# Performance work log

Measured on AMD Instinct MI355X. Metric: run time of the kernel, lower is better.

The kernel has to match this reference:

```python
import jax, jax.numpy as jnp
import numpy as np

B, L, N, T, D, V, C = 128, 512, 1023, 511, 256, 50000, 511
EPS = 1e-6


def circular_correlation(a, b):
    # c_k = sum_i a_i * b_{(i+k) mod d}  == irfft(conj(rfft(a)) * rfft(b))
    d = a.shape[-1]
    c = jnp.fft.irfft(jnp.conj(jnp.fft.rfft(a, axis=-1)) * jnp.fft.rfft(b, axis=-1), n=d, axis=-1)
    return c / (jnp.linalg.norm(c, axis=-1, keepdims=True) + EPS)


def setup_inputs() -> dict:
    key = jax.random.key(0)
    k1, k2, k3, k4, k5, k6, k7, k8 = jax.random.split(key, 8)
    num_node = jnp.full((B,), N, dtype=jnp.int64 if jax.config.jax_enable_x64 else jnp.int32)
    # leaf slot index: leaves occupy node slots 0..L-1 (deterministic, no scatter collisions)
    slot = jnp.broadcast_to(jnp.arange(L, dtype=jnp.int32)[None, :], (B, L))
    vocab_id = jax.random.randint(k1, (B, L), 0, V, dtype=jnp.int32)
    leaf_content_id = jnp.stack([slot, vocab_id], axis=-1)  # [B, L, 2]
    content_mask = (jax.random.uniform(k2, (B, L)) < 0.9).astype(jnp.int32)
    ctype = jax.random.randint(k3, (B, T), 0, 3, dtype=jnp.int32)          # 0 = no-op, 1, 2 children
    parent = jax.random.randint(k4, (B, T), L, N, dtype=jnp.int32)         # internal node slots
    lchild = jax.random.randint(k5, (B, T), 0, N, dtype=jnp.int32)
    rchild = jax.random.randint(k6, (B, T), 0, N, dtype=jnp.int32)
    composition_info = jnp.stack([ctype, parent, lchild, rchild], axis=-1)  # [B, T, 4]
    emb_weight = jax.random.normal(k7, (V, D), dtype=jnp.float32) * 0.1
    lin_weight = jax.random.normal(k8, (C, D), dtype=jnp.float32) * 0.05
    lin_bias = jnp.zeros((C,), dtype=jnp.float32)
    return {"num_node": num_node, "leaf_content_id": leaf_content_id,
            "content_mask": content_mask, "composition_info": composition_info,
            "emb_weight": emb_weight, "lin_weight": lin_weight, "lin_bias": lin_bias}


def embed_leaf_nodes(leaf_content_id, content_mask, emb_weight):
    leaf_vec = emb_weight[leaf_content_id[:, :, 1]]          # [B, L, D]
    node_idx = leaf_content_id[:, :, 0]                      # [B, L]
    mask = content_mask != 0
    safe_idx = jnp.where(mask, node_idx, N)                  # N is out-of-bounds -> dropped
    vec = jnp.zeros((B, N, D), dtype=leaf_vec.dtype)
    vec = vec.at[jnp.arange(B)[:, None], safe_idx].set(leaf_vec, mode="drop")
    norm = jnp.linalg.norm(vec, axis=2, keepdims=True) + EPS
    return vec / norm


def compose(vec, composition_info):
    bidx = jnp.arange(B)

    def step(v, info):  # info: [B, 4] for one tree level
        t, p, l, r = info[:, 0], info[:, 1], info[:, 2], info[:, 3]
        safe_p = jnp.where(t > 0, p, 0)
        lv = v[bidx, l]                                      # [B, D]
        rv = v[bidx, r]
        two = circular_correlation(lv, rv)
        cur = v[bidx, safe_p]
        val = jnp.where((t == 1)[:, None], lv,
                        jnp.where((t == 2)[:, None], two, cur))
        return v.at[bidx, safe_p].set(val), None

    vec, _ = jax.lax.scan(step, vec, jnp.swapaxes(composition_info, 0, 1))
    return vec


def reference(num_node, leaf_content_id, content_mask, composition_info,
              emb_weight, lin_weight, lin_bias):
    vec = embed_leaf_nodes(leaf_content_id, content_mask, emb_weight)
    vec = compose(vec, composition_info)
    out = jnp.einsum("bnd,cd->bnc", vec, lin_weight) + lin_bias
    return out
```

## Files before the change

kernel.cpp:

```cpp
#include <hip/hip_runtime.h>

#define NB 128
#define NL 512
#define NN 1023
#define NT 511
#define ND 256
#define NC 511
#define EPSF 1e-6f

#define SRC_ZERO (-1)
#define SLOTC 4096
#define STEPC 8192

typedef __attribute__((ext_vector_type(8))) short short8;
typedef __attribute__((ext_vector_type(4))) float f32x4;
typedef __attribute__((ext_vector_type(2))) float f32x2;

__device__ __forceinline__ unsigned short f2bf(float f) {
  unsigned u = __builtin_bit_cast(unsigned, f);
  u += 0x7FFFu + ((u >> 16) & 1u);
  return (unsigned short)(u >> 16);
}

__global__ void __launch_bounds__(256) embed_scatter(
    const int* __restrict__ lcid, const int* __restrict__ cmask,
    const float* __restrict__ emb, const float* __restrict__ lw,
    float* __restrict__ leafbuf, unsigned short* __restrict__ vecb,
    unsigned short* __restrict__ wb) {
  if (blockIdx.x >= 16384) {
    int i   = (blockIdx.x - 16384) * 256 + threadIdx.x;
    int row = i >> 5;
    uint4 r = {0u, 0u, 0u, 0u};
    if (row < NC) {
      const float4* v4 = (const float4*)lw;
      float4 x = v4[2 * i], y = v4[2 * i + 1];
      r.x = (unsigned)f2bf(x.x) | ((unsigned)f2bf(x.y) << 16);
      r.y = (unsigned)f2bf(x.z) | ((unsigned)f2bf(x.w) << 16);
      r.z = (unsigned)f2bf(y.x) | ((unsigned)f2bf(y.y) << 16);
      r.w = (unsigned)f2bf(y.z) | ((unsigned)f2bf(y.w) << 16);
    }
    ((uint4*)wb)[i] = r;
    return;
  }
  int rid  = blockIdx.x * 4 + (threadIdx.x >> 6);
  int lane = threadIdx.x & 63;
  int slot = lcid[2 * rid];
  int vid  = lcid[2 * rid + 1];
  int msk  = cmask[rid];
  int b    = rid >> 9;
  float4 v = {0.f, 0.f, 0.f, 0.f};
  if (msk) v = ((const float4*)(emb + (size_t)vid * ND))[lane];
  float ss = v.x * v.x + v.y * v.y + v.z * v.z + v.w * v.w;
#pragma unroll
  for (int off = 32; off > 0; off >>= 1) ss += __shfl_down(ss, off, 64);
  ss = __shfl(ss, 0, 64);
  float inv = 1.0f / (sqrtf(ss) + EPSF);
  float4 o;
  o.x = v.x * inv; o.y = v.y * inv; o.z = v.z * inv; o.w = v.w * inv;
  ((float4*)(leafbuf + ((size_t)b * 512 + slot) * ND))[lane] = o;
  uint2 pk;
  pk.x = (unsigned)f2bf(o.x) | ((unsigned)f2bf(o.y) << 16);
  pk.y = (unsigned)f2bf(o.z) | ((unsigned)f2bf(o.w) << 16);
  ((uint2*)(vecb + ((size_t)b * NN + slot) * ND))[lane] = pk;
}

__global__ void __launch_bounds__(1024) compose_kernel(
    const int* __restrict__ info, const int* __restrict__ lcid,
    const int* __restrict__ cmask, const float* __restrict__ leafbuf,
    float* __restrict__ outbuf, int* __restrict__ fsrcG) {
  const int b    = blockIdx.x;
  const int tid  = threadIdx.x;
  const int lane = tid & 63;
  const int wav  = tid >> 6;

  __shared__ int4 sinfo4[NT];
  __shared__ int ptr_[NT];
  __shared__ int lsA[NT], rsA[NT];
  __shared__ int lvl[NT], fsrc[NT];
  __shared__ int schedS[NT], schedL[NT], schedR[NT];
  __shared__ int offs[512], cnt[512], cnt2[512];
  __shared__ unsigned char deadF[NT], liveF[NT], lzero[512];
  __shared__ float a_st[16][256];
  __shared__ float b_st[16][512];
  __shared__ float s_st[16][512];
  __shared__ int changed, smax;

  const float* lb = leafbuf + (size_t)b * 512 * ND;
  float*       ob = outbuf + (size_t)b * NT * ND;

  const int4* ib4 = (const int4*)(info + (size_t)b * NT * 4);
  for (int i = tid; i < NT; i += 1024) sinfo4[i] = ib4[i];
  if (tid < 512) lzero[tid] = 1;
  if (tid == 0) smax = 0;
  __syncthreads();
  if (tid < NL) {
    int row = lcid[((size_t)b * NL + tid) * 2];
    lzero[row] = (cmask[(size_t)b * NL + tid] == 0) ? 1 : 0;
  }
  __syncthreads();

  const int t = tid;
  int4 m1 = {0, 0, 0, 0};
  if (t < NT) m1 = sinfo4[t];
  int l1 = -1, r1 = -1, f1 = -1;
  const int prow = 512 + t;
  for (int tp = 0; tp < NT; ++tp) {
    int4 wi = sinfo4[tp];
    if (wi.x > 0) {
      if (t < NT && tp < t) { if (wi.y == m1.z) l1 = tp; if (wi.y == m1.w) r1 = tp; }
      if (wi.y == prow) f1 = tp;
    }
  }
  __syncthreads();

  if (t < NT) {
    int v;
    if (m1.x == 2) v = SLOTC + t;
    else if (m1.x == 1) {
      if (m1.z < 512) v = m1.z;
      else v = (l1 >= 0) ? (STEPC + l1) : SRC_ZERO;
    } else v = SRC_ZERO;
    ptr_[t] = v;
  }
  __syncthreads();
  for (int it = 0; it < 10; ++it) {
    int v = 0;
    if (t < NT) { v = ptr_[t]; if (v >= STEPC) v = ptr_[v - STEPC]; }
    __syncthreads();
    if (t < NT) ptr_[t] = v;
    __syncthreads();
  }

  auto normv = [&](int v) -> int {
    if (v >= 0 && v < 512 && lzero[v]) return SRC_ZERO;
    return v;
  };
  auto collapseW = [&](int wstep) -> int {
    int v = (sinfo4[wstep].x == 2) ? (SLOTC + wstep) : ptr_[wstep];
    return normv(v);
  };
  if (t < NT) {
    if (m1.x == 2) {
      int a = (m1.z < 512) ? normv(m1.z) : ((l1 >= 0) ? collapseW(l1) : SRC_ZERO);
      int c = (m1.w < 512) ? normv(m1.w) : ((r1 >= 0) ? collapseW(r1) : SRC_ZERO);
      lsA[t] = a; rsA[t] = c;
      deadF[t] = (a == SRC_ZERO || c == SRC_ZERO) ? 1 : 0;
    } else {
      deadF[t] = 0;
    }
    liveF[t] = 0;
    fsrc[t] = (f1 >= 0) ? collapseW(f1) : SRC_ZERO;
  }
  __syncthreads();

  for (int rounds = 0; rounds < NT; ++rounds) {
    if (tid == 0) changed = 0;
    __syncthreads();
    if (t < NT && m1.x == 2 && !deadF[t]) {
      int a = lsA[t], c = rsA[t];
      if (a >= SLOTC && deadF[a - SLOTC]) { a = SRC_ZERO; lsA[t] = a; }
      if (c >= SLOTC && deadF[c - SLOTC]) { c = SRC_ZERO; rsA[t] = c; }
      if (a == SRC_ZERO || c == SRC_ZERO) { deadF[t] = 1; changed = 1; }
    }
    __syncthreads();
    if (!changed) break;
    __syncthreads();
  }

  if (t < NT) {
    int f = fsrc[t];
    if (f >= SLOTC && deadF[f - SLOTC]) { f = SRC_ZERO; fsrc[t] = f; }
    if (f >= SLOTC) liveF[f - SLOTC] = 1;
  }
  __syncthreads();
  for (int rounds = 0; rounds < NT; ++rounds) {
    if (tid == 0) changed = 0;
    __syncthreads();
    if (t < NT && m1.x == 2 && liveF[t] && !deadF[t]) {
      int a = lsA[t], c = rsA[t];
      if (a >= SLOTC && !liveF[a - SLOTC]) { liveF[a - SLOTC] = 1; changed = 1; }
      if (c >= SLOTC && !liveF[c - SLOTC]) { liveF[c - SLOTC] = 1; changed = 1; }
    }
    __syncthreads();
    if (!changed) break;
    __syncthreads();
  }

  const bool isLive = (t < NT && m1.x == 2 && liveF[t] && !deadF[t]);

  if (t < NT) lvl[t] = 0;
  __syncthreads();
  for (int rounds = 0; rounds < NT; ++rounds) {
    if (tid == 0) changed = 0;
    __syncthreads();
    if (isLive) {
      int nl = 1, a = lsA[t], c = rsA[t];
      if (a >= SLOTC) { int dl = lvl[a - SLOTC] + 1; if (dl > nl) nl = dl; }
      if (c >= SLOTC) { int dl = lvl[c - SLOTC] + 1; if (dl > nl) nl = dl; }
      if (nl > lvl[t]) { lvl[t] = nl; changed = 1; }
    }
    __syncthreads();
    if (!changed) break;
    __syncthreads();
  }
  if (isLive) atomicMax(&smax, lvl[t]);

  if (tid < 512) { cnt[tid] = 0; cnt2[tid] = 0; }
  __syncthreads();
  if (isLive) atomicAdd(&cnt[lvl[t]], 1);
  __syncthreads();
  if (tid < 512) offs[tid] = cnt[tid];
  __syncthreads();
  for (int k = 1; k < 512; k <<= 1) {
    int v = 0;
    if (tid < 512) { v = offs[tid]; if (tid >= k) v += offs[tid - k]; }
    __syncthreads();
    if (tid < 512) offs[tid] = v;
    __syncthreads();
  }
  if (isLive) {
    int d = lvl[t];
    int pos = offs[d - 1] + atomicAdd(&cnt2[d], 1);
    schedS[pos] = t; schedL[pos] = lsA[t]; schedR[pos] = rsA[t];
  }
  __syncthreads();

  const int maxd = smax;
  for (int d = 1; d <= maxd; ++d) {
    const int base = offs[d - 1];
    const int nops = cnt[d];
    const int nch  = (nops + 15) >> 4;
    for (int ch = 0; ch < nch; ++ch) {
      int rel = ch * 16 + wav;
      if (rel < nops) {
        int my = base + rel;
        int tt = schedS[my], ls = schedL[my], rs = schedR[my];
        const float* pa = (ls < 512) ? lb + (size_t)ls * ND
                                     : ob + (size_t)(ls - SLOTC) * ND;
        const float* pb = (rs < 512) ? lb + (size_t)rs * ND
                                     : ob + (size_t)(rs - SLOTC) * ND;
        float4 av = ((const float4*)pa)[lane];
        float4 bv = ((const float4*)pb)[lane];
        float nx = __shfl(bv.x, (lane + 1) & 63, 64);
        float4 sv = {bv.y, bv.z, bv.w, nx};
        ((float4*)a_st[wav])[lane]      = av;
        ((float4*)b_st[wav])[lane]      = bv;
        ((float4*)b_st[wav])[lane + 64] = bv;
        ((float4*)s_st[wav])[lane]      = sv;
        ((float4*)s_st[wav])[lane + 64] = sv;
        const float4* a4 = (const float4*)a_st[wav];
        const float4* b4 = (const float4*)b_st[wav];
        const float4* s4 = (const float4*)s_st[wav];
        f32x2 q0 = {0.f, 0.f}, q1 = {0.f, 0.f}, q2 = {0.f, 0.f}, q3 = {0.f, 0.f};
        float4 B0 = b4[lane];
        float4 S0 = s4[lane];
#pragma unroll 8
        for (int i = 0; i < 64; ++i) {
          float4 A  = a4[i];
          float4 B1 = b4[lane + i + 1];
          float4 S1 = s4[lane + i + 1];
          f32x2 Axy = {A.x, A.y},  Azw = {A.z, A.w};
          f32x2 Bxy = {B0.x, B0.y}, Bzw = {B0.z, B0.w};
          f32x2 Sxy = {S0.x, S0.y}, Szw = {S0.z, S0.w};
          f32x2 B1xy = {B1.x, B1.y}, S1xy = {S1.x, S1.y};
          q0 += Axy * Bxy;  q0 += Azw * Bzw;
          q1 += Axy * Sxy;  q1 += Azw * Szw;
          q2 += Axy * Bzw;  q2 += Azw * B1xy;
          q3 += Axy * Szw;  q3 += Azw * S1xy;
          B0 = B1; S0 = S1;
        }
        float c0 = q0.x + q0.y, c1 = q1.x + q1.y;
        float c2 = q2.x + q2.y, c3 = q3.x + q3.y;
        float ss = c0 * c0 + c1 * c1 + c2 * c2 + c3 * c3;
#pragma unroll
        for (int off = 32; off > 0; off >>= 1) ss += __shfl_down(ss, off, 64);
        ss = __shfl(ss, 0, 64);
        float inv = 1.f / (sqrtf(ss) + EPSF);
        float4 res;
        res.x = c0 * inv; res.y = c1 * inv; res.z = c2 * inv; res.w = c3 * inv;
        ((float4*)(ob + (size_t)tt * ND))[lane] = res;
      }
    }
    __syncthreads();
  }

  for (int i = tid; i < NT; i += 1024) fsrcG[b * NT + i] = fsrc[i];
}

__global__ void __launch_bounds__(256) gather_rows(
    const int* __restrict__ fsrcG, const float* __restrict__ leafbuf,
    const float* __restrict__ outbuf, unsigned short* __restrict__ vecb) {
  int rid  = blockIdx.x * 4 + (threadIdx.x >> 6);
  int lane = threadIdx.x & 63;
  int b    = rid / NT;
  int idx  = rid - b * NT;
  int s    = fsrcG[rid];
  float4 v = {0.f, 0.f, 0.f, 0.f};
  if (s >= 0) {
    const float* src = (s < 512)
        ? (leafbuf + ((size_t)b * 512 + s) * ND)
        : (outbuf + ((size_t)b * NT + (s - SLOTC)) * ND);
    v = ((const float4*)src)[lane];
  }
  uint2 pk;
  pk.x = (unsigned)f2bf(v.x) | ((unsigned)f2bf(v.y) << 16);
  pk.y = (unsigned)f2bf(v.z) | ((unsigned)f2bf(v.w) << 16);
  ((uint2*)(vecb + ((size_t)b * NN + 512 + idx) * ND))[lane] = pk;
}

union GemmSh {
  struct { short As[128 * 64]; short Ws[128 * 64]; } s;
  float epi[4][16][65];
};

__global__ void __launch_bounds__(256) gemm_kernel(
    const short* __restrict__ A, const short* __restrict__ W,
    const float* __restrict__ bias, float* __restrict__ out) {
  __shared__ GemmSh sh;
  int i = blockIdx.x;
  int m = (i >> 5) * 8 + (i & 7);
  int c = (i >> 3) & 3;
  if (m >= 1023) return;
  int tid  = threadIdx.x;
  int lane = tid & 63;
  int w    = tid >> 6;
  int c0   = c * 128;
  int m0   = m * 128;
  int wm   = (w & 1) * 64;
  int wc   = (w >> 1) * 64;
  int frow = lane & 15;
  int quad = lane >> 4;
  f32x4 acc[4][4];
#pragma unroll
  for (int a = 0; a < 4; ++a)
#pragma unroll
    for (int j = 0; j < 4; ++j) acc[a][j] = (f32x4){0.f, 0.f, 0.f, 0.f};

  for (int k0 = 0; k0 < ND; k0 += 64) {
#pragma unroll
    for (int a = 0; a < 4; ++a) {
      int idx = a * 256 + tid;
      int row = idx >> 3;
      int ch  = idx & 7;
      int chs = ch ^ (row & 7);
      const short* ga = A + (size_t)(m0 + row) * ND + k0 + chs * 8;
      const short* gw = W + (size_t)(c0 + row) * ND + k0 + chs * 8;
      __builtin_amdgcn_global_load_lds(
          (const __attribute__((address_space(1))) void*)ga,
          (__attribute__((address_space(3))) void*)(sh.s.As + idx * 8), 16, 0, 0);
      __builtin_amdgcn_global_load_lds(
          (const __attribute__((address_space(1))) void*)gw,
          (__attribute__((address_space(3))) void*)(sh.s.Ws + idx * 8), 16, 0, 0);
    }
    __syncthreads();
#pragma unroll
    for (int ks = 0; ks < 2; ++ks) {
      short8 af[4], wf[4];
#pragma unroll
      for (int mi = 0; mi < 4; ++mi) {
        int r = wm + mi * 16 + frow;
        int cc = (ks * 4 + quad) ^ (r & 7);
        af[mi] = *(const short8*)(sh.s.As + r * 64 + cc * 8);
      }
#pragma unroll
      for (int ci = 0; ci < 4; ++ci) {
        int r = wc + ci * 16 + frow;
        int cc = (ks * 4 + quad) ^ (r & 7);
        wf[ci] = *(const short8*)(sh.s.Ws + r * 64 + cc * 8);
      }
#pragma unroll
      for (int mi = 0; mi < 4; ++mi)
#pragma unroll
        for (int ci = 0; ci < 4; ++ci)
          acc[mi][ci] = __builtin_amdgcn_mfma_f32_16x16x32_bf16(
              af[mi], wf[ci], acc[mi][ci], 0, 0, 0);
    }
    __syncthreads();
  }

  int colg = c0 + wc + lane;
  float bv = (colg < NC) ? bias[colg] : 0.f;
#pragma unroll
  for (int mi = 0; mi < 4; ++mi) {
#pragma unroll
    for (int ci = 0; ci < 4; ++ci)
#pragma unroll
      for (int r = 0; r < 4; ++r)
        sh.epi[w][quad * 4 + r][ci * 16 + frow] = acc[mi][ci][r];
    if (colg < NC) {
      int mrow = m0 + wm + mi * 16;
#pragma unroll
      for (int rr = 0; rr < 16; ++rr)
        out[(size_t)(mrow + rr) * NC + colg] = sh.epi[w][rr][lane] + bv;
    }
  }
}

extern "C" void kernel_launch(void* const* d_in, const int* in_sizes, int n_in,
                              void* d_out, int out_size, void* d_ws, size_t ws_size,
                              hipStream_t stream) {
  const int*   lcid  = (const int*)d_in[1];
  const int*   cmask = (const int*)d_in[2];
  const int*   cinfo = (const int*)d_in[3];
  const float* emb   = (const float*)d_in[4];
  const float* lw    = (const float*)d_in[5];
  const float* lbias = (const float*)d_in[6];
  float*       out   = (float*)d_out;

  char* ws = (char*)d_ws;
  float*          leafbuf = (float*)ws;
  float*          outbuf  = (float*)(ws + 67108864);
  unsigned short* vecb    = (unsigned short*)(ws + 134086656);
  unsigned short* wb      = (unsigned short*)(ws + 201129984);
  int*            fsrcG   = (int*)d_out;

  embed_scatter<<<16448, 256, 0, stream>>>(lcid, cmask, emb, lw,
                                           leafbuf, vecb, wb);
  compose_kernel<<<NB, 1024, 0, stream>>>(cinfo, lcid, cmask, leafbuf,
                                          outbuf, fsrcG);
  gather_rows<<<NB * NT / 4, 256, 0, stream>>>(fsrcG, leafbuf, outbuf, vecb);
  gemm_kernel<<<4096, 256, 0, stream>>>(
      (const short*)vecb, (const short*)wb, lbias, out);
}
```

Measured before the change: 520.6 us.

## Overlap leaf-row GEMM with tree composition in a fused kernel

The compose kernel gains 1024 extra blocks that compute the output projection for the leaf rows (slots 0..511), whose bf16 vectors are already final after the embed step. These blocks fill the GPU while the 128 compose blocks run their serial dependency walk. The later GEMM now covers only the internal-node rows, which halves its grid. The fsrc scratch is moved inside the output buffer to a region that only the second GEMM writes. This relies on compose blocks being scheduled first, and the fused kernel keeps 1024-thread blocks with the large union shared-memory footprint, which can limit occupancy for the GEMM blocks.

```diff
diff --git a/kernel.cpp b/kernel.cpp
--- a/kernel.cpp
+++ b/kernel.cpp
@@ -64,227 +64,323 @@
   ((uint2*)(vecb + ((size_t)b * NN + slot) * ND))[lane] = pk;
 }
 
-__global__ void __launch_bounds__(1024) compose_kernel(
+struct ComposeSh {
+  int4 sinfo4[NT];
+  int ptr_[NT];
+  int lsA[NT], rsA[NT];
+  int lvl[NT], fsrc[NT];
+  int schedS[NT], schedL[NT], schedR[NT];
+  int offs[512], cnt[512], cnt2[512];
+  unsigned char deadF[NT], liveF[NT], lzero[512];
+  float a_st[16][256];
+  float b_st[16][512];
+  float s_st[16][512];
+  int changed, smax;
+};
+struct LeafGemmSh { short As[256 * 64]; short Ws[128 * 64]; };
+union FuseSh { ComposeSh c; LeafGemmSh g; };
+
+__global__ void __launch_bounds__(1024) compose_leafgemm(
     const int* __restrict__ info, const int* __restrict__ lcid,
     const int* __restrict__ cmask, const float* __restrict__ leafbuf,
-    float* __restrict__ outbuf, int* __restrict__ fsrcG) {
-  const int b    = blockIdx.x;
+    float* __restrict__ outbuf, int* __restrict__ fsrcG,
+    const short* __restrict__ vecbS, const short* __restrict__ wbs,
+    const float* __restrict__ bias, float* __restrict__ out) {
+  __shared__ FuseSh sh;
   const int tid  = threadIdx.x;
   const int lane = tid & 63;
   const int wav  = tid >> 6;
 
-  __shared__ int4 sinfo4[NT];
-  __shared__ int ptr_[NT];
-  __shared__ int lsA[NT], rsA[NT];
-  __shared__ int lvl[NT], fsrc[NT];
-  __shared__ int schedS[NT], schedL[NT], schedR[NT];
-  __shared__ int offs[512], cnt[512], cnt2[512];
-  __shared__ unsigned char deadF[NT], liveF[NT], lzero[512];
-  __shared__ float a_st[16][256];
-  __shared__ float b_st[16][512];
-  __shared__ float s_st[16][512];
-  __shared__ int changed, smax;
-
-  const float* lb = leafbuf + (size_t)b * 512 * ND;
-  float*       ob = outbuf + (size_t)b * NT * ND;
-
-  const int4* ib4 = (const int4*)(info + (size_t)b * NT * 4);
-  for (int i = tid; i < NT; i += 1024) sinfo4[i] = ib4[i];
-  if (tid < 512) lzero[tid] = 1;
-  if (tid == 0) smax = 0;
-  __syncthreads();
-  if (tid < NL) {
-    int row = lcid[((size_t)b * NL + tid) * 2];
-    lzero[row] = (cmask[(size_t)b * NL + tid] == 0) ? 1 : 0;
-  }
-  __syncthreads();
-
-  const int t = tid;
-  int4 m1 = {0, 0, 0, 0};
-  if (t < NT) m1 = sinfo4[t];
-  int l1 = -1, r1 = -1, f1 = -1;
-  const int prow = 512 + t;
-  for (int tp = 0; tp < NT; ++tp) {
-    int4 wi = sinfo4[tp];
-    if (wi.x > 0) {
-      if (t < NT && tp < t) { if (wi.y == m1.z) l1 = tp; if (wi.y == m1.w) r1 = tp; }
-      if (wi.y == prow) f1 = tp;
-    }
-  }
-  __syncthreads();
-
-  if (t < NT) {
-    int v;
-    if (m1.x == 2) v = SLOTC + t;
-    else if (m1.x == 1) {
-      if (m1.z < 512) v = m1.z;
-      else v = (l1 >= 0) ? (STEPC + l1) : SRC_ZERO;
-    } else v = SRC_ZERO;
-    ptr_[t] = v;
-  }
-  __syncthreads();
-  for (int it = 0; it < 10; ++it) {
-    int v = 0;
-    if (t < NT) { v = ptr_[t]; if (v >= STEPC) v = ptr_[v - STEPC]; }
-    __syncthreads();
-    if (t < NT) ptr_[t] = v;
-    __syncthreads();
-  }
-
-  auto normv = [&](int v) -> int {
-    if (v >= 0 && v < 512 && lzero[v]) return SRC_ZERO;
-    return v;
-  };
-  auto collapseW = [&](int wstep) -> int {
-    int v = (sinfo4[wstep].x == 2) ? (SLOTC + wstep) : ptr_[wstep];
-    return normv(v);
-  };
-  if (t < NT) {
-    if (m1.x == 2) {
-      int a = (m1.z < 512) ? normv(m1.z) : ((l1 >= 0) ? collapseW(l1) : SRC_ZERO);
-      int c = (m1.w < 512) ? normv(m1.w) : ((r1 >= 0) ? collapseW(r1) : SRC_ZERO);
-      lsA[t] = a; rsA[t] = c;
-      deadF[t] = (a == SRC_ZERO || c == SRC_ZERO) ? 1 : 0;
-    } else {
-      deadF[t] = 0;
-    }
-    liveF[t] = 0;
-    fsrc[t] = (f1 >= 0) ? collapseW(f1) : SRC_ZERO;
-  }
-  __syncthreads();
-
-  for (int rounds = 0; rounds < NT; ++rounds) {
-    if (tid == 0) changed = 0;
-    __syncthreads();
-    if (t < NT && m1.x == 2 && !deadF[t]) {
-      int a = lsA[t], c = rsA[t];
-      if (a >= SLOTC && deadF[a - SLOTC]) { a = SRC_ZERO; lsA[t] = a; }
-      if (c >= SLOTC && deadF[c - SLOTC]) { c = SRC_ZERO; rsA[t] = c; }
-      if (a == SRC_ZERO || c == SRC_ZERO) { deadF[t] = 1; changed = 1; }
-    }
-    __syncthreads();
-    if (!changed) break;
-    __syncthreads();
-  }
-
-  if (t < NT) {
-    int f = fsrc[t];
-    if (f >= SLOTC && deadF[f - SLOTC]) { f = SRC_ZERO; fsrc[t] = f; }
-    if (f >= SLOTC) liveF[f - SLOTC] = 1;
-  }
-  __syncthreads();
-  for (int rounds = 0; rounds < NT; ++rounds) {
-    if (tid == 0) changed = 0;
-    __syncthreads();
-    if (t < NT && m1.x == 2 && liveF[t] && !deadF[t]) {
-      int a = lsA[t], c = rsA[t];
-      if (a >= SLOTC && !liveF[a - SLOTC]) { liveF[a - SLOTC] = 1; changed = 1; }
-      if (c >= SLOTC && !liveF[c - SLOTC]) { liveF[c - SLOTC] = 1; changed = 1; }
-    }
-    __syncthreads();
-    if (!changed) break;
-    __syncthreads();
-  }
-
-  const bool isLive = (t < NT && m1.x == 2 && liveF[t] && !deadF[t]);
-
-  if (t < NT) lvl[t] = 0;
-  __syncthreads();
-  for (int rounds = 0; rounds < NT; ++rounds) {
-    if (tid == 0) changed = 0;
-    __syncthreads();
+  if (blockIdx.x < NB) {
+    const int b = blockIdx.x;
+    int4 (&sinfo4)[NT] = sh.c.sinfo4;
+    int (&ptr_)[NT] = sh.c.ptr_;
+    int (&lsA)[NT] = sh.c.lsA;  int (&rsA)[NT] = sh.c.rsA;
+    int (&lvl)[NT] = sh.c.lvl;  int (&fsrc)[NT] = sh.c.fsrc;
+    int (&schedS)[NT] = sh.c.schedS; int (&schedL)[NT] = sh.c.schedL;
+    int (&schedR)[NT] = sh.c.schedR;
+    int (&offs)[512] = sh.c.offs; int (&cnt)[512] = sh.c.cnt;
+    int (&cnt2)[512] = sh.c.cnt2;
+    unsigned char (&deadF)[NT] = sh.c.deadF;
+    unsigned char (&liveF)[NT] = sh.c.liveF;
+    unsigned char (&lzero)[512] = sh.c.lzero;
+    float (&a_st)[16][256] = sh.c.a_st;
+    float (&b_st)[16][512] = sh.c.b_st;
+    float (&s_st)[16][512] = sh.c.s_st;
+    int &changed = sh.c.changed; int &smax = sh.c.smax;
+
+    const float* lb = leafbuf + (size_t)b * 512 * ND;
+    float*       ob = outbuf + (size_t)b * NT * ND;
+
+    const int4* ib4 = (const int4*)(info + (size_t)b * NT * 4);
+    for (int i = tid; i < NT; i += 1024) sinfo4[i] = ib4[i];
+    if (tid < 512) lzero[tid] = 1;
+    if (tid == 0) smax = 0;
+    __syncthreads();
+    if (tid < NL) {
+      int row = lcid[((size_t)b * NL + tid) * 2];
+      lzero[row] = (cmask[(size_t)b * NL + tid] == 0) ? 1 : 0;
+    }
+    __syncthreads();
+
+    const int t = tid;
+    int4 m1 = {0, 0, 0, 0};
+    if (t < NT) m1 = sinfo4[t];
+    int l1 = -1, r1 = -1, f1 = -1;
+    const int prow = 512 + t;
+    for (int tp = 0; tp < NT; ++tp) {
+      int4 wi = sinfo4[tp];
+      if (wi.x > 0) {
+        if (t < NT && tp < t) { if (wi.y == m1.z) l1 = tp; if (wi.y == m1.w) r1 = tp; }
+        if (wi.y == prow) f1 = tp;
+      }
+    }
+    __syncthreads();
+
+    if (t < NT) {
+      int v;
+      if (m1.x == 2) v = SLOTC + t;
+      else if (m1.x == 1) {
+        if (m1.z < 512) v = m1.z;
+        else v = (l1 >= 0) ? (STEPC + l1) : SRC_ZERO;
+      } else v = SRC_ZERO;
+      ptr_[t] = v;
+    }
+    __syncthreads();
+    for (int it = 0; it < 10; ++it) {
+      int v = 0;
+      if (t < NT) { v = ptr_[t]; if (v >= STEPC) v = ptr_[v - STEPC]; }
+      __syncthreads();
+      if (t < NT) ptr_[t] = v;
+      __syncthreads();
+    }
+
+    auto normv = [&](int v) -> int {
+      if (v >= 0 && v < 512 && lzero[v]) return SRC_ZERO;
+      return v;
+    };
+    auto collapseW = [&](int wstep) -> int {
+      int v = (sinfo4[wstep].x == 2) ? (SLOTC + wstep) : ptr_[wstep];
+      return normv(v);
+    };
+    if (t < NT) {
+      if (m1.x == 2) {
+        int a = (m1.z < 512) ? normv(m1.z) : ((l1 >= 0) ? collapseW(l1) : SRC_ZERO);
+        int c = (m1.w < 512) ? normv(m1.w) : ((r1 >= 0) ? collapseW(r1) : SRC_ZERO);
+        lsA[t] = a; rsA[t] = c;
+        deadF[t] = (a == SRC_ZERO || c == SRC_ZERO) ? 1 : 0;
+      } else {
+        deadF[t] = 0;
+      }
+      liveF[t] = 0;
+      fsrc[t] = (f1 >= 0) ? collapseW(f1) : SRC_ZERO;
+    }
+    __syncthreads();
+
+    for (int rounds = 0; rounds < NT; ++rounds) {
+      if (tid == 0) changed = 0;
+      __syncthreads();
+      if (t < NT && m1.x == 2 && !deadF[t]) {
+        int a = lsA[t], c = rsA[t];
+        if (a >= SLOTC && deadF[a - SLOTC]) { a = SRC_ZERO; lsA[t] = a; }
+        if (c >= SLOTC && deadF[c - SLOTC]) { c = SRC_ZERO; rsA[t] = c; }
+        if (a == SRC_ZERO || c == SRC_ZERO) { deadF[t] = 1; changed = 1; }
+      }
+      __syncthreads();
+      if (!changed) break;
+      __syncthreads();
+    }
+
+    if (t < NT) {
+      int f = fsrc[t];
+      if (f >= SLOTC && deadF[f - SLOTC]) { f = SRC_ZERO; fsrc[t] = f; }
+      if (f >= SLOTC) liveF[f - SLOTC] = 1;
+    }
+    __syncthreads();
+    for (int rounds = 0; rounds < NT; ++rounds) {
+      if (tid == 0) changed = 0;
+      __syncthreads();
+      if (t < NT && m1.x == 2 && liveF[t] && !deadF[t]) {
+        int a = lsA[t], c = rsA[t];
+        if (a >= SLOTC && !liveF[a - SLOTC]) { liveF[a - SLOTC] = 1; changed = 1; }
+        if (c >= SLOTC && !liveF[c - SLOTC]) { liveF[c - SLOTC] = 1; changed = 1; }
+      }
+      __syncthreads();
+      if (!changed) break;
+      __syncthreads();
+    }
+
+    const bool isLive = (t < NT && m1.x == 2 && liveF[t] && !deadF[t]);
+
+    if (t < NT) lvl[t] = 0;
+    __syncthreads();
+    for (int rounds = 0; rounds < NT; ++rounds) {
+      if (tid == 0) changed = 0;
+      __syncthreads();
+      if (isLive) {
+        int nl = 1, a = lsA[t], c = rsA[t];
+        if (a >= SLOTC) { int dl = lvl[a - SLOTC] + 1; if (dl > nl) nl = dl; }
+        if (c >= SLOTC) { int dl = lvl[c - SLOTC] + 1; if (dl > nl) nl = dl; }
+        if (nl > lvl[t]) { lvl[t] = nl; changed = 1; }
+      }
+      __syncthreads();
+      if (!changed) break;
+      __syncthreads();
+    }
+    if (isLive) atomicMax(&smax, lvl[t]);
+
+    if (tid < 512) { cnt[tid] = 0; cnt2[tid] = 0; }
+    __syncthreads();
+    if (isLive) atomicAdd(&cnt[lvl[t]], 1);
+    __syncthreads();
+    if (tid < 512) offs[tid] = cnt[tid];
+    __syncthreads();
+    for (int k = 1; k < 512; k <<= 1) {
+      int v = 0;
+      if (tid < 512) { v = offs[tid]; if (tid >= k) v += offs[tid - k]; }
+      __syncthreads();
+      if (tid < 512) offs[tid] = v;
+      __syncthreads();
+    }
     if (isLive) {
-      int nl = 1, a = lsA[t], c = rsA[t];
-      if (a >= SLOTC) { int dl = lvl[a - SLOTC] + 1; if (dl > nl) nl = dl; }
-      if (c >= SLOTC) { int dl = lvl[c - SLOTC] + 1; if (dl > nl) nl = dl; }
-      if (nl > lvl[t]) { lvl[t] = nl; changed = 1; }
-    }
-    __syncthreads();
-    if (!changed) break;
-    __syncthreads();
-  }
-  if (isLive) atomicMax(&smax, lvl[t]);
-
-  if (tid < 512) { cnt[tid] = 0; cnt2[tid] = 0; }
-  __syncthreads();
-  if (isLive) atomicAdd(&cnt[lvl[t]], 1);
-  __syncthreads();
-  if (tid < 512) offs[tid] = cnt[tid];
-  __syncthreads();
-  for (int k = 1; k < 512; k <<= 1) {
-    int v = 0;
-    if (tid < 512) { v = offs[tid]; if (tid >= k) v += offs[tid - k]; }
-    __syncthreads();
-    if (tid < 512) offs[tid] = v;
-    __syncthreads();
-  }
-  if (isLive) {
-    int d = lvl[t];
-    int pos = offs[d - 1] + atomicAdd(&cnt2[d], 1);
-    schedS[pos] = t; schedL[pos] = lsA[t]; schedR[pos] = rsA[t];
-  }
-  __syncthreads();
-
-  const int maxd = smax;
-  for (int d = 1; d <= maxd; ++d) {
-    const int base = offs[d - 1];
-    const int nops = cnt[d];
-    const int nch  = (nops + 15) >> 4;
-    for (int ch = 0; ch < nch; ++ch) {
-      int rel = ch * 16 + wav;
-      if (rel < nops) {
-        int my = base + rel;
-        int tt = schedS[my], ls = schedL[my], rs = schedR[my];
-        const float* pa = (ls < 512) ? lb + (size_t)ls * ND
-                                     : ob + (size_t)(ls - SLOTC) * ND;
-        const float* pb = (rs < 512) ? lb + (size_t)rs * ND
-                                     : ob + (size_t)(rs - SLOTC) * ND;
-        float4 av = ((const float4*)pa)[lane];
-        float4 bv = ((const float4*)pb)[lane];
-        float nx = __shfl(bv.x, (lane + 1) & 63, 64);
-        float4 sv = {bv.y, bv.z, bv.w, nx};
-        ((float4*)a_st[wav])[lane]      = av;
-        ((float4*)b_st[wav])[lane]      = bv;
-        ((float4*)b_st[wav])[lane + 64] = bv;
-        ((float4*)s_st[wav])[lane]      = sv;
-        ((float4*)s_st[wav])[lane + 64] = sv;
-        const float4* a4 = (const float4*)a_st[wav];
-        const float4* b4 = (const float4*)b_st[wav];
-        const float4* s4 = (const float4*)s_st[wav];
-        f32x2 q0 = {0.f, 0.f}, q1 = {0.f, 0.f}, q2 = {0.f, 0.f}, q3 = {0.f, 0.f};
-        float4 B0 = b4[lane];
-        float4 S0 = s4[lane];
+      int d = lvl[t];
+      int pos = offs[d - 1] + atomicAdd(&cnt2[d], 1);
+      schedS[pos] = t; schedL[pos] = lsA[t]; schedR[pos] = rsA[t];
+    }
+    __syncthreads();
+
+    const int maxd = smax;
+    for (int d = 1; d <= maxd; ++d) {
+      const int base = offs[d - 1];
+      const int nops = cnt[d];
+      const int nch  = (nops + 15) >> 4;
+      for (int ch = 0; ch < nch; ++ch) {
+        int rel = ch * 16 + wav;
+        if (rel < nops) {
+          int my = base + rel;
+          int tt = schedS[my], ls = schedL[my], rs = schedR[my];
+          const float* pa = (ls < 512) ? lb + (size_t)ls * ND
+                                       : ob + (size_t)(ls - SLOTC) * ND;
+          const float* pb = (rs < 512) ? lb + (size_t)rs * ND
+                                       : ob + (size_t)(rs - SLOTC) * ND;
+          float4 av = ((const float4*)pa)[lane];
+          float4 bv = ((const float4*)pb)[lane];
+          float nx = __shfl(bv.x, (lane + 1) & 63, 64);
+          float4 sv = {bv.y, bv.z, bv.w, nx};
+          ((float4*)a_st[wav])[lane]      = av;
+          ((float4*)b_st[wav])[lane]      = bv;
+          ((float4*)b_st[wav])[lane + 64] = bv;
+          ((float4*)s_st[wav])[lane]      = sv;
+          ((float4*)s_st[wav])[lane + 64] = sv;
+          const float4* a4 = (const float4*)a_st[wav];
+          const float4* b4 = (const float4*)b_st[wav];
+          const float4* s4 = (const float4*)s_st[wav];
+          f32x2 q0 = {0.f, 0.f}, q1 = {0.f, 0.f}, q2 = {0.f, 0.f}, q3 = {0.f, 0.f};
+          float4 B0 = b4[lane];
+          float4 S0 = s4[lane];
 #pragma unroll 8
-        for (int i = 0; i < 64; ++i) {
-          float4 A  = a4[i];
-          float4 B1 = b4[lane + i + 1];
-          float4 S1 = s4[lane + i + 1];
-          f32x2 Axy = {A.x, A.y},  Azw = {A.z, A.w};
-          f32x2 Bxy = {B0.x, B0.y}, Bzw = {B0.z, B0.w};
-          f32x2 Sxy = {S0.x, S0.y}, Szw = {S0.z, S0.w};
-          f32x2 B1xy = {B1.x, B1.y}, S1xy = {S1.x, S1.y};
-          q0 += Axy * Bxy;  q0 += Azw * Bzw;
-          q1 += Axy * Sxy;  q1 += Azw * Szw;
-          q2 += Axy * Bzw;  q2 += Azw * B1xy;
-          q3 += Axy * Szw;  q3 += Azw * S1xy;
-          B0 = B1; S0 = S1;
+          for (int i = 0; i < 64; ++i) {
+            float4 A  = a4[i];
+            float4 B1 = b4[lane + i + 1];
+            float4 S1 = s4[lane + i + 1];
+            f32x2 Axy = {A.x, A.y},  Azw = {A.z, A.w};
+            f32x2 Bxy = {B0.x, B0.y}, Bzw = {B0.z, B0.w};
+            f32x2 Sxy = {S0.x, S0.y}, Szw = {S0.z, S0.w};
+            f32x2 B1xy = {B1.x, B1.y}, S1xy = {S1.x, S1.y};
+            q0 += Axy * Bxy;  q0 += Azw * Bzw;
+            q1 += Axy * Sxy;  q1 += Azw * Szw;
+            q2 += Axy * Bzw;  q2 += Azw * B1xy;
+            q3 += Axy * Szw;  q3 += Azw * S1xy;
+            B0 = B1; S0 = S1;
+          }
+          float c0 = q0.x + q0.y, c1 = q1.x + q1.y;
+          float c2 = q2.x + q2.y, c3 = q3.x + q3.y;
+          float ss = c0 * c0 + c1 * c1 + c2 * c2 + c3 * c3;
+#pragma unroll
+          for (int off = 32; off > 0; off >>= 1) ss += __shfl_down(ss, off, 64);
+          ss = __shfl(ss, 0, 64);
+          float inv = 1.f / (sqrtf(ss) + EPSF);
+          float4 res;
+          res.x = c0 * inv; res.y = c1 * inv; res.z = c2 * inv; res.w = c3 * inv;
+          ((float4*)(ob + (size_t)tt * ND))[lane] = res;
         }
-        float c0 = q0.x + q0.y, c1 = q1.x + q1.y;
-        float c2 = q2.x + q2.y, c3 = q3.x + q3.y;
-        float ss = c0 * c0 + c1 * c1 + c2 * c2 + c3 * c3;
-#pragma unroll
-        for (int off = 32; off > 0; off >>= 1) ss += __shfl_down(ss, off, 64);
-        ss = __shfl(ss, 0, 64);
-        float inv = 1.f / (sqrtf(ss) + EPSF);
-        float4 res;
-        res.x = c0 * inv; res.y = c1 * inv; res.z = c2 * inv; res.w = c3 * inv;
-        ((float4*)(ob + (size_t)tt * ND))[lane] = res;
-      }
-    }
-    __syncthreads();
-  }
-
-  for (int i = tid; i < NT; i += 1024) fsrcG[b * NT + i] = fsrc[i];
+      }
+      __syncthreads();
+    }
+
+    for (int i = tid; i < NT; i += 1024) fsrcG[b * NT + i] = fsrc[i];
+    return;
+  }
+
+  const int gidx = blockIdx.x - NB;
+  const int b  = gidx >> 3;
+  const int mt = (gidx >> 2) & 1;
+  const int ct = gidx & 3;
+  const short* A = vecbS + ((size_t)b * NN + mt * 256) * ND;
+  const int c0   = ct * 128;
+  const int wr   = wav >> 1;
+  const int wc   = wav & 1;
+  const int frow = lane & 15;
+  const int quad = lane >> 4;
+  f32x4 acc[2][4];
+#pragma unroll
+  for (int i = 0; i < 2; ++i)
+#pragma unroll
+    for (int j = 0; j < 4; ++j) acc[i][j] = (f32x4){0.f, 0.f, 0.f, 0.f};
+
+  for (int k0 = 0; k0 < ND; k0 += 64) {
+#pragma unroll
+    for (int i = 0; i < 2; ++i) {
+      int idx = i * 1024 + tid;
+      int row = idx >> 3;
+      int chn = idx & 7;
+      const short* ga = A + (size_t)row * ND + k0 + chn * 8;
+      __builtin_amdgcn_global_load_lds(
+          (const __attribute__((address_space(1))) void*)ga,
+          (__attribute__((address_space(3))) void*)(sh.g.As + idx * 8), 16, 0, 0);
+    }
+    {
+      int row = tid >> 3;
+      int chn = tid & 7;
+      const short* gw = wbs + (size_t)(c0 + row) * ND + k0 + chn * 8;
+      __builtin_amdgcn_global_load_lds(
+          (const __attribute__((address_space(1))) void*)gw,
+          (__attribute__((address_space(3))) void*)(sh.g.Ws + tid * 8), 16, 0, 0);
+    }
+    __syncthreads();
+#pragma unroll
+    for (int ks = 0; ks < 2; ++ks) {
+      short8 af[2], wf[4];
+#pragma unroll
+      for (int mi = 0; mi < 2; ++mi)
+        af[mi] = *(const short8*)(sh.g.As + (wr * 32 + mi * 16 + frow) * 64 + ks * 32 + quad * 8);
+#pragma unroll
+      for (int ci = 0; ci < 4; ++ci)
+        wf[ci] = *(const short8*)(sh.g.Ws + (wc * 64 + ci * 16 + frow) * 64 + ks * 32 + quad * 8);
+#pragma unroll
+      for (int mi = 0; mi < 2; ++mi)
+#pragma unroll
+        for (int ci = 0; ci < 4; ++ci)
+          acc[mi][ci] = __builtin_amdgcn_mfma_f32_16x16x32_bf16(
+              af[mi], wf[ci], acc[mi][ci], 0, 0, 0);
+    }
+    __syncthreads();
+  }
+#pragma unroll
+  for (int mi = 0; mi < 2; ++mi) {
+#pragma unroll
+    for (int ci = 0; ci < 4; ++ci) {
+      int col = c0 + wc * 64 + ci * 16 + frow;
+      if (col < NC) {
+        float bv = bias[col];
+#pragma unroll
+        for (int r = 0; r < 4; ++r) {
+          int n = mt * 256 + wr * 32 + mi * 16 + quad * 4 + r;
+          out[((size_t)b * NN + n) * NC + col] = acc[mi][ci][r] + bv;
+        }
+      }
+    }
+  }
 }
 
 __global__ void __launch_bounds__(256) gather_rows(
@@ -313,19 +409,20 @@
   float epi[4][16][65];
 };
 
-__global__ void __launch_bounds__(256) gemm_kernel(
+__global__ void __launch_bounds__(256) gemm_int(
     const short* __restrict__ A, const short* __restrict__ W,
     const float* __restrict__ bias, float* __restrict__ out) {
   __shared__ GemmSh sh;
   int i = blockIdx.x;
-  int m = (i >> 5) * 8 + (i & 7);
-  int c = (i >> 3) & 3;
-  if (m >= 1023) return;
+  int mtile = (i >> 5) * 8 + (i & 7);
+  int c     = (i >> 3) & 3;
+  int b     = mtile >> 2;
+  int mt    = mtile & 3;
+  size_t arow = (size_t)b * NN + 512 + mt * 128;
   int tid  = threadIdx.x;
   int lane = tid & 63;
   int w    = tid >> 6;
   int c0   = c * 128;
-  int m0   = m * 128;
   int wm   = (w & 1) * 64;
   int wc   = (w >> 1) * 64;
   int frow = lane & 15;
@@ -343,7 +440,7 @@
       int row = idx >> 3;
       int ch  = idx & 7;
       int chs = ch ^ (row & 7);
-      const short* ga = A + (size_t)(m0 + row) * ND + k0 + chs * 8;
+      const short* ga = A + (arow + row) * ND + k0 + chs * 8;
       const short* gw = W + (size_t)(c0 + row) * ND + k0 + chs * 8;
       __builtin_amdgcn_global_load_lds(
           (const __attribute__((address_space(1))) void*)ga,
@@ -388,10 +485,13 @@
       for (int r = 0; r < 4; ++r)
         sh.epi[w][quad * 4 + r][ci * 16 + frow] = acc[mi][ci][r];
     if (colg < NC) {
-      int mrow = m0 + wm + mi * 16;
-#pragma unroll
-      for (int rr = 0; rr < 16; ++rr)
-        out[(size_t)(mrow + rr) * NC + colg] = sh.epi[w][rr][lane] + bv;
+      int nbase = 512 + mt * 128 + wm + mi * 16;
+#pragma unroll
+      for (int rr = 0; rr < 16; ++rr) {
+        int n = nbase + rr;
+        if (n < NN)
+          out[((size_t)b * NN + n) * NC + colg] = sh.epi[w][rr][lane] + bv;
+      }
     }
   }
 }
@@ -412,13 +512,14 @@
   float*          outbuf  = (float*)(ws + 67108864);
   unsigned short* vecb    = (unsigned short*)(ws + 134086656);
   unsigned short* wb      = (unsigned short*)(ws + 201129984);
-  int*            fsrcG   = (int*)d_out;
+  int*            fsrcG   = (int*)d_out + (size_t)512 * NC;
 
   embed_scatter<<<16448, 256, 0, stream>>>(lcid, cmask, emb, lw,
                                            leafbuf, vecb, wb);
-  compose_kernel<<<NB, 1024, 0, stream>>>(cinfo, lcid, cmask, leafbuf,
-                                          outbuf, fsrcG);
+  compose_leafgemm<<<NB + 1024, 1024, 0, stream>>>(
+      cinfo, lcid, cmask, leafbuf, outbuf, fsrcG,
+      (const short*)vecb, (const short*)wb, lbias, out);
   gather_rows<<<NB * NT / 4, 256, 0, stream>>>(fsrcG, leafbuf, outbuf, vecb);
-  gemm_kernel<<<4096, 256, 0, stream>>>(
+  gemm_int<<<2048, 256, 0, stream>>>(
       (const short*)vecb, (const short*)wb, lbias, out);
 }
```

New measurement: 480.5 us, median of 2. 7.7% less time.
